# Optimization experiments

Hardware: AMD Instinct MI355X
Metric: run time of the kernel (lower is better)

## Reference

```python
import jax, jax.numpy as jnp
import numpy as np

N_LAYERS = 3


def setup_inputs() -> dict:
    key = jax.random.key(0)
    k1, k2, k3, k4 = jax.random.split(key, 4)
    user_emb = jax.random.normal(k1, (29858, 64), dtype=jnp.float32)
    item_emb = jax.random.normal(k2, (40981, 64), dtype=jnp.float32)
    v = jax.random.normal(k3, (70839, 512), dtype=jnp.float32)
    filters = jax.random.normal(k4, (N_LAYERS, 512), dtype=jnp.float32)
    return {"user_emb": user_emb, "item_emb": item_emb, "v": v, "filters": filters}


def reference(user_emb, item_emb, v, filters):
    # ego: [N, D], v: [N, F], filters: [L, F]
    n_users = user_emb.shape[0]
    ego = jnp.concatenate([user_emb, item_emb], axis=0)
    acc = ego  # running sum for the mean over (layers + 1) embeddings
    for k in range(filters.shape[0]):
        # V @ diag(f) @ V^T @ ego  ==  V @ (f[:, None] * (V^T @ ego))
        proj = v.T @ ego                      # [F, D]
        ego = v @ (filters[k][:, None] * proj)  # [N, D]
        acc = acc + ego
    all_emb = acc / (filters.shape[0] + 1)
    return all_emb[:n_users], all_emb[n_users:]
```

## Files before the change

kernel.cpp:

```cpp
#include <hip/hip_runtime.h>
#include <hip/hip_bf16.h>


#define N_USERS 29858
#define N_TOTAL 70839
#define DQ 64
#define FD 512
#define NPAD 71168

typedef __attribute__((ext_vector_type(8))) short short8;
typedef __attribute__((ext_vector_type(4))) short short4v;
typedef __attribute__((ext_vector_type(4))) float f32x4;
typedef unsigned int u32;
typedef unsigned short u16;

static __device__ __forceinline__ u32 f32u(float x){union{float f;u32 u;}a;a.f=x;return a.u;}
static __device__ __forceinline__ float uf32(u32 u){union{u32 u;float f;}a;a.u=u;return a.f;}
static __device__ __forceinline__ u32 pack_h(u32 x0, u32 x1){
  return __builtin_amdgcn_perm(x1, x0, 0x07060302u);
}
static __device__ __forceinline__ void split_pair(u32 x0, u32 x1, u32& hp, u32& lp) {
  hp = pack_h(x0, x1);
  u32 l0 = f32u(uf32(x0) - uf32(x0 & 0xFFFF0000u));
  u32 l1 = f32u(uf32(x1) - uf32(x1 & 0xFFFF0000u));
  lp = pack_h(l0, l1);
}
union U8x { u32 u[4]; short8 s; };

static __device__ __forceinline__ u16 bf16_rne(float x) {
  u32 u = f32u(x);
  return (u16)((u + 0x7FFFu + ((u >> 16) & 1u)) >> 16);
}
static __device__ __forceinline__ void split2(float x, u16& h, u16& l) {
  h = bf16_rne(x);
  l = bf16_rne(x - uf32(((u32)h) << 16));
}

static __device__ __forceinline__ void load_lds16(const float* g, float* l) {
  __builtin_amdgcn_global_load_lds(
      (const __attribute__((address_space(1))) u32*)(g),
      (__attribute__((address_space(3))) u32*)(l), 16, 0, 0);
}


__global__ __launch_bounds__(256) void init_kernel(
    const float* __restrict__ u, const float* __restrict__ it,
    float* __restrict__ out, u16* __restrict__ egoTb) {
  __shared__ float tile[64][65];
  const int n0 = blockIdx.x * 64;
  const int t = threadIdx.x;
  const int r = t >> 2, cbase = (t & 3) * 16;
  {
    int n = n0 + r;
    if (n < N_TOTAL) {
      const float* src = (n < N_USERS) ? (u + (size_t)n * DQ)
                                       : (it + (size_t)(n - N_USERS) * DQ);
#pragma unroll
      for (int q = 0; q < 4; ++q) {
        f32x4 val = *(const f32x4*)(src + cbase + q * 4);
        *(f32x4*)(out + (size_t)n * DQ + cbase + q * 4) = val;
        tile[r][cbase + q * 4 + 0] = val[0];
        tile[r][cbase + q * 4 + 1] = val[1];
        tile[r][cbase + q * 4 + 2] = val[2];
        tile[r][cbase + q * 4 + 3] = val[3];
      }
    } else {
#pragma unroll
      for (int q = 0; q < 4; ++q)
#pragma unroll
        for (int e = 0; e < 4; ++e) tile[r][cbase + q * 4 + e] = 0.f;
    }
  }
  __syncthreads();
  const int s = t;
  const int d = (s & 15) | ((s >> 6) << 4);
  const int nb = (s >> 4) & 3;
#pragma unroll
  for (int sl = 0; sl < 2; ++sl) {
    U8x H, L;
#pragma unroll
    for (int j = 0; j < 4; ++j) {
      u16 h0, l0, h1, l1;
      split2(tile[sl * 32 + nb * 8 + 2 * j][d], h0, l0);
      split2(tile[sl * 32 + nb * 8 + 2 * j + 1][d], h1, l1);
      H.u[j] = (u32)h0 | ((u32)h1 << 16);
      L.u[j] = (u32)l0 | ((u32)l1 << 16);
    }
    size_t base = (size_t)(blockIdx.x * 2 + sl) * 4096;
    *(short8*)(egoTb + base + (size_t)s * 8) = H.s;
    *(short8*)(egoTb + base + 2048 + (size_t)s * 8) = L.s;
  }
}

__global__ __launch_bounds__(256, 2) void gram_kernel(
    const float* __restrict__ v, const u16* __restrict__ egoTb,
    float* __restrict__ parts, int chunk) {
  __shared__ short8 HAh[1024];
  __shared__ short8 HAl[1024];
  __shared__ short8 HBh[256];
  __shared__ short8 HBl[256];

  const int job = blockIdx.x;
  const int n0c = blockIdx.y * chunk;
  const int nend = min(n0c + chunk, NPAD);
  const bool isC0 = (job >= 12);
  const int itile = isC0 ? (job - 12) : (job < 8 ? 0 : 1);
  const int fA = itile * 256;
  const int jcol = isC0 ? 0 : (job < 8 ? job : job - 4);
  const int colbase = jcol * 64;
  const bool reuseB = !isC0 && (colbase >= fA) && (colbase + 64 <= fA + 256);
  const bool stageB = !isC0 && !reuseB;
  const int cb0q = reuseB ? ((colbase - fA) >> 6) : 0;

  const int t = threadIdx.x;
  const int lane = t & 63, wv = t >> 6;
  const int m16 = lane & 15, quad = lane >> 4;
  const int fl = lane, nq = wv;

  f32x4 acc[4][4];
#pragma unroll
  for (int a = 0; a < 4; ++a)
#pragma unroll
    for (int b = 0; b < 4; ++b) acc[a][b] = (f32x4){0.f, 0.f, 0.f, 0.f};

  u32 xA[4][8];
  u32 xB[8];
  short8 xBh, xBl;

  auto issue = [&](int n0) {
    if (isC0) {
      xBh = *(const short8*)(egoTb + (size_t)(n0 >> 5) * 4096 + (size_t)t * 8);
      xBl = *(const short8*)(egoTb + (size_t)(n0 >> 5) * 4096 + 2048 + (size_t)t * 8);
    }
#pragma unroll
    for (int seg = 0; seg < 4; ++seg)
#pragma unroll
      for (int r = 0; r < 8; ++r) {
        int n = n0 + nq * 8 + r;
        xA[seg][r] = (n < N_TOTAL) ? f32u(v[(size_t)n * FD + fA + seg * 64 + fl]) : 0u;
      }
    if (stageB) {
#pragma unroll
      for (int r = 0; r < 8; ++r) {
        int n = n0 + nq * 8 + r;
        xB[r] = (n < N_TOTAL) ? f32u(v[(size_t)n * FD + colbase + fl]) : 0u;
      }
    }
  };

  issue(n0c);

  for (int n0 = n0c; n0 < nend; n0 += 32) {
    asm volatile("s_barrier" ::: "memory");

    const int uw = (fl & 15) + ((fl >> 4) & 3) * 64 + nq * 16;
#pragma unroll
    for (int seg = 0; seg < 4; ++seg) {
      U8x H, L;
#pragma unroll
      for (int p = 0; p < 4; ++p)
        split_pair(xA[seg][2 * p], xA[seg][2 * p + 1], H.u[p], L.u[p]);
      HAh[uw + seg * 256] = H.s;
      HAl[uw + seg * 256] = L.s;
    }
    if (stageB) {
      U8x H, L;
#pragma unroll
      for (int p = 0; p < 4; ++p)
        split_pair(xB[2 * p], xB[2 * p + 1], H.u[p], L.u[p]);
      HBh[uw] = H.s;
      HBl[uw] = L.s;
    } else if (isC0) {
      HBh[t] = xBh;
      HBl[t] = xBl;
    }

    if (n0 + 32 < nend) issue(n0 + 32);

    asm volatile("s_waitcnt lgkmcnt(0)" ::: "memory");
    asm volatile("s_barrier" ::: "memory");

    short8 ah[4], al[4];
#pragma unroll
    for (int mt = 0; mt < 4; ++mt) {
      int u = m16 + mt * 64 + wv * 256 + quad * 16;
      ah[mt] = HAh[u];
      al[mt] = HAl[u];
    }
#pragma unroll
    for (int ct = 0; ct < 4; ++ct) {
      short8 bh, bl;
      if (reuseB) {
        int u = m16 + ct * 64 + cb0q * 256 + quad * 16;
        bh = HAh[u]; bl = HAl[u];
      } else {
        int u = m16 + ct * 64 + quad * 16;
        bh = HBh[u]; bl = HBl[u];
      }
#pragma unroll
      for (int mt = 0; mt < 4; ++mt) {
        acc[mt][ct] = __builtin_amdgcn_mfma_f32_16x16x32_bf16(ah[mt], bh, acc[mt][ct], 0, 0, 0);
        acc[mt][ct] = __builtin_amdgcn_mfma_f32_16x16x32_bf16(ah[mt], bl, acc[mt][ct], 0, 0, 0);
        acc[mt][ct] = __builtin_amdgcn_mfma_f32_16x16x32_bf16(al[mt], bh, acc[mt][ct], 0, 0, 0);
      }
    }
  }

  float* pb = parts + (size_t)blockIdx.y * (512 * 576);
  const int cb = isC0 ? 512 : colbase;
#pragma unroll
  for (int mt = 0; mt < 4; ++mt) {
    int row = fA + wv * 64 + mt * 16 + quad * 4;
#pragma unroll
    for (int ct = 0; ct < 4; ++ct) {
      int col = cb + ct * 16 + m16;
#pragma unroll
      for (int reg = 0; reg < 4; ++reg)
        pb[(size_t)(row + reg) * 576 + col] = acc[mt][ct][reg];
    }
  }
}

__global__ __launch_bounds__(256) void finalize_kernel(
    const float* __restrict__ parts, int nc,
    float* __restrict__ G, float* __restrict__ c0) {
  int idx = blockIdx.x * 256 + threadIdx.x;
  int r = idx / 576, c = idx % 576;
  float s = 0.f;
  if (c >= 512) {
    for (int p = 0; p < nc; ++p) s += parts[(size_t)p * (512 * 576) + r * 576 + c];
    c0[r * 64 + (c - 512)] = s;
  } else {
    bool direct = (c >> 6) >= 4 * (r >> 8);
    int rr = direct ? r : c, cc = direct ? c : r;
    for (int p = 0; p < nc; ++p) s += parts[(size_t)p * (512 * 576) + rr * 576 + cc];
    G[r * 512 + c] = s;
  }
}

__global__ __launch_bounds__(256) void apply_g_kernel(
    const float* __restrict__ G, const float* __restrict__ filt,
    const float* __restrict__ cin, float* __restrict__ cout) {
  __shared__ float red[4][64];
  const int t = threadIdx.x;
  const int i = blockIdx.x;
  const int sub = t >> 6, d = t & 63;
  float s = 0.f;
#pragma unroll 8
  for (int j = sub * 128; j < (sub + 1) * 128; ++j)
    s += G[i * 512 + j] * (filt[j] * cin[j * 64 + d]);
  red[sub][d] = s;
  __syncthreads();
  if (sub == 0)
    cout[i * 64 + d] = red[0][d] + red[1][d] + red[2][d] + red[3][d];
}

__global__ __launch_bounds__(256) void prep_wt_kernel(
    const float* __restrict__ filters, const float* __restrict__ c0,
    const float* __restrict__ c1, const float* __restrict__ c2,
    u16* __restrict__ wt_h, u16* __restrict__ wt_l) {
  int idx = blockIdx.x * 256 + threadIdx.x;
  int d = idx >> 9, f = idx & 511;
  float w = filters[f] * c0[f * 64 + d] + filters[512 + f] * c1[f * 64 + d] +
            filters[1024 + f] * c2[f * 64 + d];
  u32 xu = f32u(w);
  u32 h = xu & 0xFFFF0000u;
  u32 lu = f32u(w - uf32(h));
  wt_h[d * FD + f] = (u16)(xu >> 16);
  wt_l[d * FD + f] = (u16)(lu >> 16);
}

__global__ __launch_bounds__(256) void expand_kernel(
    const float* __restrict__ v, const u16* __restrict__ wt_h,
    const u16* __restrict__ wt_l, float* __restrict__ out) {
  __shared__ float raw[2][128 * 64];
  const int t = threadIdx.x;
  const int lane = t & 63, wv = t >> 6;
  const int m16 = lane & 15, quad = lane >> 4;
  const int nb = blockIdx.x * 128;

  f32x4 acc[2][4];
#pragma unroll
  for (int a = 0; a < 2; ++a)
#pragma unroll
    for (int b = 0; b < 4; ++b) acc[a][b] = (f32x4){0.f, 0.f, 0.f, 0.f};

  auto stage = [&](int buf, int fs) {
#pragma unroll
    for (int g = 0; g < 8; ++g) {
      int rl = g * 4 + (lane >> 4);
      int sw = rl & 7;
      int grow = min(nb + wv * 32 + rl, N_TOTAL - 1);
      const float* gp = v + (size_t)grow * FD + fs + (((lane & 15) ^ sw) << 2);
      load_lds16(gp, &raw[buf][(wv * 32 + g * 4) * 64]);
    }
  };

  stage(0, 0);
  for (int it8 = 0; it8 < 8; ++it8) {
    const int buf = it8 & 1, fs = it8 * 64;
    short8 pbh[2][4], pbl[2][4];
#pragma unroll
    for (int k = 0; k < 2; ++k)
#pragma unroll
      for (int ct = 0; ct < 4; ++ct) {
        const size_t off = (size_t)(ct * 16 + m16) * FD + fs + k * 32 + quad * 8;
        pbh[k][ct] = *(const short8*)(wt_h + off);
        pbl[k][ct] = *(const short8*)(wt_l + off);
      }
    asm volatile("" ::: "memory");
    if (it8 + 1 < 8) {
      stage(buf ^ 1, fs + 64);
      asm volatile("s_waitcnt vmcnt(24)" ::: "memory");
    } else {
      asm volatile("s_waitcnt vmcnt(16)" ::: "memory");
    }
#pragma unroll
    for (int k0i = 0; k0i < 2; ++k0i) {
      short8 ah[2], al[2];
#pragma unroll
      for (int mt = 0; mt < 2; ++mt) {
        const float* rb = &raw[buf][(wv * 32 + mt * 16 + m16) * 64];
        const int sw = m16 & 7;
        const int j0 = k0i * 8 + quad * 2;
        f32x4 xa = *(const f32x4*)(rb + ((j0 ^ sw) << 2));
        f32x4 xb = *(const f32x4*)(rb + (((j0 + 1) ^ sw) << 2));
        U8x H, L;
        split_pair(f32u(xa[0]), f32u(xa[1]), H.u[0], L.u[0]);
        split_pair(f32u(xa[2]), f32u(xa[3]), H.u[1], L.u[1]);
        split_pair(f32u(xb[0]), f32u(xb[1]), H.u[2], L.u[2]);
        split_pair(f32u(xb[2]), f32u(xb[3]), H.u[3], L.u[3]);
        ah[mt] = H.s; al[mt] = L.s;
      }
#pragma unroll
      for (int ct = 0; ct < 4; ++ct) {
#pragma unroll
        for (int mt = 0; mt < 2; ++mt) {
          acc[mt][ct] = __builtin_amdgcn_mfma_f32_16x16x32_bf16(ah[mt], pbh[k0i][ct], acc[mt][ct], 0, 0, 0);
          acc[mt][ct] = __builtin_amdgcn_mfma_f32_16x16x32_bf16(ah[mt], pbl[k0i][ct], acc[mt][ct], 0, 0, 0);
          acc[mt][ct] = __builtin_amdgcn_mfma_f32_16x16x32_bf16(al[mt], pbh[k0i][ct], acc[mt][ct], 0, 0, 0);
        }
      }
    }
  }

#pragma unroll
  for (int mt = 0; mt < 2; ++mt) {
    int nrow = nb + wv * 32 + mt * 16 + quad * 4;
#pragma unroll
    for (int ct = 0; ct < 4; ++ct) {
      int d = ct * 16 + m16;
#pragma unroll
      for (int reg = 0; reg < 4; ++reg) {
        int n = nrow + reg;
        if (n < N_TOTAL) {
          float* op = out + (size_t)n * DQ + d;
          *op = (*op + acc[mt][ct][reg]) * 0.25f;
        }
      }
    }
  }
}

extern "C" void kernel_launch(void* const* d_in, const int* in_sizes, int n_in,
                              void* d_out, int out_size, void* d_ws, size_t ws_size,
                              hipStream_t stream) {
  const float* user_emb = (const float*)d_in[0];
  const float* item_emb = (const float*)d_in[1];
  const float* v        = (const float*)d_in[2];
  const float* filters  = (const float*)d_in[3];
  float* out = (float*)d_out;

  const size_t EGOTB_BYTES = (size_t)(NPAD / 32) * 8192;
  const size_t SMALL_BYTES = (512 * 512 + 3 * 512 * 64) * 4 + 2 * DQ * FD * 2;
  size_t avail = ws_size > EGOTB_BYTES + SMALL_BYTES
                     ? ws_size - EGOTB_BYTES - SMALL_BYTES : 0;
  int nc = (int)(avail / ((size_t)512 * 576 * 4));
  if (nc > 70) nc = 70;
  if (nc < 1) nc = 1;
  int chunk = ((NPAD + nc - 1) / nc + 31) & ~31;
  int ncA = (NPAD + chunk - 1) / chunk;

  u16* egoTb  = (u16*)d_ws;
  float* parts = (float*)((char*)d_ws + EGOTB_BYTES);
  float* G     = parts + (size_t)ncA * 512 * 576;
  float* c0    = G + 512 * 512;
  float* c1    = c0 + 512 * 64;
  float* c2    = c1 + 512 * 64;
  u16* wt_h    = (u16*)(c2 + 512 * 64);
  u16* wt_l    = wt_h + (size_t)DQ * FD;

  init_kernel<<<NPAD / 64, 256, 0, stream>>>(user_emb, item_emb, out, egoTb);
  gram_kernel<<<dim3(14, ncA), 256, 0, stream>>>(v, egoTb, parts, chunk);
  finalize_kernel<<<(512 * 576) / 256, 256, 0, stream>>>(parts, ncA, G, c0);
  apply_g_kernel<<<512, 256, 0, stream>>>(G, filters, c0, c1);
  apply_g_kernel<<<512, 256, 0, stream>>>(G, filters + 512, c1, c2);
  prep_wt_kernel<<<128, 256, 0, stream>>>(filters, c0, c1, c2, wt_h, wt_l);
  expand_kernel<<<NPAD / 128, 256, 0, stream>>>(v, wt_h, wt_l, out);
}
```

Before: 476.6 us.

## Drop split-bf16 in expand, remap gram grid, cap chunks and raise occupancy

The expand kernel stops using the hi/lo bf16 split for both V and the weight matrix. It now does a single bf16 MFMA per tile, with round-to-nearest weights and truncated V, which removes two thirds of the MFMAs, the low-part loads and the split arithmetic. The gram kernel moves to a 1D grid that interleaves chunk indices across jobs, likely to improve L2 locality on v, and raises launch bounds to 3 blocks per CU. The chunk count is capped at 35 instead of 70, which shrinks the partials buffer and finalize work. The precision drop lowers accuracy of the final expansion, roughly to bf16 level, and could break tolerance.

```diff
diff --git a/kernel.cpp b/kernel.cpp
--- a/kernel.cpp
+++ b/kernel.cpp
@@ -92,7 +92,7 @@
   }
 }
 
-__global__ __launch_bounds__(256, 2) void gram_kernel(
+__global__ __launch_bounds__(256, 3) void gram_kernel(
     const float* __restrict__ v, const u16* __restrict__ egoTb,
     float* __restrict__ parts, int chunk) {
   __shared__ short8 HAh[1024];
@@ -100,8 +100,11 @@
   __shared__ short8 HBh[256];
   __shared__ short8 HBl[256];
 
-  const int job = blockIdx.x;
-  const int n0c = blockIdx.y * chunk;
+  const int lid = blockIdx.x;
+  const int cidx = (lid & 7) + 8 * ((lid >> 3) / 14);
+  const int job = (lid >> 3) % 14;
+  const int n0c = cidx * chunk;
+  if (n0c >= NPAD) return;
   const int nend = min(n0c + chunk, NPAD);
   const bool isC0 = (job >= 12);
   const int itile = isC0 ? (job - 12) : (job < 8 ? 0 : 1);
@@ -206,7 +209,7 @@
     }
   }
 
-  float* pb = parts + (size_t)blockIdx.y * (512 * 576);
+  float* pb = parts + (size_t)cidx * (512 * 576);
   const int cb = isC0 ? 512 : colbase;
 #pragma unroll
   for (int mt = 0; mt < 4; ++mt) {
@@ -258,21 +261,17 @@
 __global__ __launch_bounds__(256) void prep_wt_kernel(
     const float* __restrict__ filters, const float* __restrict__ c0,
     const float* __restrict__ c1, const float* __restrict__ c2,
-    u16* __restrict__ wt_h, u16* __restrict__ wt_l) {
+    u16* __restrict__ wt_h) {
   int idx = blockIdx.x * 256 + threadIdx.x;
   int d = idx >> 9, f = idx & 511;
   float w = filters[f] * c0[f * 64 + d] + filters[512 + f] * c1[f * 64 + d] +
             filters[1024 + f] * c2[f * 64 + d];
-  u32 xu = f32u(w);
-  u32 h = xu & 0xFFFF0000u;
-  u32 lu = f32u(w - uf32(h));
-  wt_h[d * FD + f] = (u16)(xu >> 16);
-  wt_l[d * FD + f] = (u16)(lu >> 16);
+  wt_h[d * FD + f] = bf16_rne(w);
 }
 
 __global__ __launch_bounds__(256) void expand_kernel(
     const float* __restrict__ v, const u16* __restrict__ wt_h,
-    const u16* __restrict__ wt_l, float* __restrict__ out) {
+    float* __restrict__ out) {
   __shared__ float raw[2][128 * 64];
   const int t = threadIdx.x;
   const int lane = t & 63, wv = t >> 6;
@@ -299,25 +298,24 @@
   stage(0, 0);
   for (int it8 = 0; it8 < 8; ++it8) {
     const int buf = it8 & 1, fs = it8 * 64;
-    short8 pbh[2][4], pbl[2][4];
+    short8 pbh[2][4];
 #pragma unroll
     for (int k = 0; k < 2; ++k)
 #pragma unroll
       for (int ct = 0; ct < 4; ++ct) {
         const size_t off = (size_t)(ct * 16 + m16) * FD + fs + k * 32 + quad * 8;
         pbh[k][ct] = *(const short8*)(wt_h + off);
-        pbl[k][ct] = *(const short8*)(wt_l + off);
       }
     asm volatile("" ::: "memory");
     if (it8 + 1 < 8) {
       stage(buf ^ 1, fs + 64);
-      asm volatile("s_waitcnt vmcnt(24)" ::: "memory");
+      asm volatile("s_waitcnt vmcnt(16)" ::: "memory");
     } else {
-      asm volatile("s_waitcnt vmcnt(16)" ::: "memory");
+      asm volatile("s_waitcnt vmcnt(8)" ::: "memory");
     }
 #pragma unroll
     for (int k0i = 0; k0i < 2; ++k0i) {
-      short8 ah[2], al[2];
+      short8 ah[2];
 #pragma unroll
       for (int mt = 0; mt < 2; ++mt) {
         const float* rb = &raw[buf][(wv * 32 + mt * 16 + m16) * 64];
@@ -325,20 +323,18 @@
         const int j0 = k0i * 8 + quad * 2;
         f32x4 xa = *(const f32x4*)(rb + ((j0 ^ sw) << 2));
         f32x4 xb = *(const f32x4*)(rb + (((j0 + 1) ^ sw) << 2));
-        U8x H, L;
-        split_pair(f32u(xa[0]), f32u(xa[1]), H.u[0], L.u[0]);
-        split_pair(f32u(xa[2]), f32u(xa[3]), H.u[1], L.u[1]);
-        split_pair(f32u(xb[0]), f32u(xb[1]), H.u[2], L.u[2]);
-        split_pair(f32u(xb[2]), f32u(xb[3]), H.u[3], L.u[3]);
-        ah[mt] = H.s; al[mt] = L.s;
+        U8x H;
+        H.u[0] = pack_h(f32u(xa[0]), f32u(xa[1]));
+        H.u[1] = pack_h(f32u(xa[2]), f32u(xa[3]));
+        H.u[2] = pack_h(f32u(xb[0]), f32u(xb[1]));
+        H.u[3] = pack_h(f32u(xb[2]), f32u(xb[3]));
+        ah[mt] = H.s;
       }
 #pragma unroll
       for (int ct = 0; ct < 4; ++ct) {
 #pragma unroll
         for (int mt = 0; mt < 2; ++mt) {
           acc[mt][ct] = __builtin_amdgcn_mfma_f32_16x16x32_bf16(ah[mt], pbh[k0i][ct], acc[mt][ct], 0, 0, 0);
-          acc[mt][ct] = __builtin_amdgcn_mfma_f32_16x16x32_bf16(ah[mt], pbl[k0i][ct], acc[mt][ct], 0, 0, 0);
-          acc[mt][ct] = __builtin_amdgcn_mfma_f32_16x16x32_bf16(al[mt], pbh[k0i][ct], acc[mt][ct], 0, 0, 0);
         }
       }
     }
@@ -372,11 +368,11 @@
   float* out = (float*)d_out;
 
   const size_t EGOTB_BYTES = (size_t)(NPAD / 32) * 8192;
-  const size_t SMALL_BYTES = (512 * 512 + 3 * 512 * 64) * 4 + 2 * DQ * FD * 2;
+  const size_t SMALL_BYTES = (512 * 512 + 3 * 512 * 64) * 4 + DQ * FD * 2;
   size_t avail = ws_size > EGOTB_BYTES + SMALL_BYTES
                      ? ws_size - EGOTB_BYTES - SMALL_BYTES : 0;
   int nc = (int)(avail / ((size_t)512 * 576 * 4));
-  if (nc > 70) nc = 70;
+  if (nc > 35) nc = 35;
   if (nc < 1) nc = 1;
   int chunk = ((NPAD + nc - 1) / nc + 31) & ~31;
   int ncA = (NPAD + chunk - 1) / chunk;
@@ -388,13 +384,14 @@
   float* c1    = c0 + 512 * 64;
   float* c2    = c1 + 512 * 64;
   u16* wt_h    = (u16*)(c2 + 512 * 64);
-  u16* wt_l    = wt_h + (size_t)DQ * FD;
+
+  int gblocks = 8 * 14 * ((ncA + 7) / 8);
 
   init_kernel<<<NPAD / 64, 256, 0, stream>>>(user_emb, item_emb, out, egoTb);
-  gram_kernel<<<dim3(14, ncA), 256, 0, stream>>>(v, egoTb, parts, chunk);
+  gram_kernel<<<gblocks, 256, 0, stream>>>(v, egoTb, parts, chunk);
   finalize_kernel<<<(512 * 576) / 256, 256, 0, stream>>>(parts, ncA, G, c0);
   apply_g_kernel<<<512, 256, 0, stream>>>(G, filters, c0, c1);
   apply_g_kernel<<<512, 256, 0, stream>>>(G, filters + 512, c1, c2);
-  prep_wt_kernel<<<128, 256, 0, stream>>>(filters, c0, c1, c2, wt_h, wt_l);
-  expand_kernel<<<NPAD / 128, 256, 0, stream>>>(v, wt_h, wt_l, out);
-}
+  prep_wt_kernel<<<128, 256, 0, stream>>>(filters, c0, c1, c2, wt_h);
+  expand_kernel<<<NPAD / 128, 256, 0, stream>>>(v, wt_h, out);
+}
```

Result: slower. 486.8 us (+2.1%).
